# Performance work log

Measured on AMD Instinct MI355X. Metric: run time of the kernel, lower is better.

The kernel has to match this reference:

```python
import jax, jax.numpy as jnp
import numpy as np

B, S, D = 2, 2048, 1024
H = 16
HD = D // H  # 64

def setup_inputs() -> dict:
    key = jax.random.key(0)
    ks = jax.random.split(key, 5)
    scale = 0.02
    x = jax.random.normal(ks[0], (B, S, D), dtype=jnp.float32)
    w_attn = jax.random.normal(ks[1], (D, 3 * D), dtype=jnp.float32) * scale
    b_attn = jnp.zeros((3 * D,), dtype=jnp.float32)
    w_proj = jax.random.normal(ks[2], (D, D), dtype=jnp.float32) * scale
    b_proj = jnp.zeros((D,), dtype=jnp.float32)
    return {"x": x, "w_attn": w_attn, "b_attn": b_attn, "w_proj": w_proj, "b_proj": b_proj}

def reference(x, w_attn, b_attn, w_proj, b_proj):
    b, s, d = x.shape
    qkv = x @ w_attn + b_attn                      # [B,S,3D]
    q, k, v = jnp.split(qkv, 3, axis=-1)
    # [B,H,S,HD]
    q = q.reshape(b, s, H, HD).transpose(0, 2, 1, 3)
    k = k.reshape(b, s, H, HD).transpose(0, 2, 1, 3)
    v = v.reshape(b, s, H, HD).transpose(0, 2, 1, 3)
    scores = jnp.einsum('bhqd,bhkd->bhqk', q, k) * (1.0 / np.sqrt(HD))
    causal = jnp.tril(jnp.ones((s, s), dtype=bool))
    scores = jnp.where(causal[None, None], scores, -jnp.inf)
    attn = jax.nn.softmax(scores, axis=-1)
    out = jnp.einsum('bhqk,bhkd->bhqd', attn, v)   # [B,H,S,HD]
    out = out.transpose(0, 2, 1, 3).reshape(b, s, d)
    return out @ w_proj + b_proj
```

## Files before the change

### kernel.cpp

```cpp
#include <hip/hip_runtime.h>

#define B_  2
#define S_  2048
#define D_  1024
#define H_  16
#define HD_ 64
#define TD_ 3072
#define M_  (B_*S_)
#define NWORK_ 24

using bf16x8 = __attribute__((ext_vector_type(8))) short;
using bf16x4 = __attribute__((ext_vector_type(4))) short;
using f32x4  = __attribute__((ext_vector_type(4))) float;

typedef __attribute__((address_space(1))) unsigned int uint_g;
typedef __attribute__((address_space(3))) unsigned int uint_l;

#define MFMA32 __builtin_amdgcn_mfma_f32_16x16x32_bf16

#if defined(__has_builtin)
#if __has_builtin(__builtin_amdgcn_mfma_f32_16x16x16_bf16_1k)
#define MFMA16(a,b,c) __builtin_amdgcn_mfma_f32_16x16x16_bf16_1k(a,b,c,0,0,0)
#define HAVE_MFMA16 1
#elif __has_builtin(__builtin_amdgcn_mfma_f32_16x16x16bf16_1k)
#define MFMA16(a,b,c) __builtin_amdgcn_mfma_f32_16x16x16bf16_1k(a,b,c,0,0,0)
#define HAVE_MFMA16 1
#endif
#endif
#ifndef HAVE_MFMA16
static __device__ __forceinline__ f32x4 MFMA16_stub(bf16x4 a, bf16x4 b, f32x4 c) { return c; }
#define MFMA16(a,b,c) MFMA16_stub(a,b,c)
#endif

static __device__ __forceinline__ short f2bf(float f) {
    unsigned u = __float_as_uint(f);
    u += 0x7FFFu + ((u >> 16) & 1u);
    return (short)(u >> 16);
}
static __device__ __forceinline__ unsigned pack2bf(float a, float b) {
    return (unsigned)(unsigned short)f2bf(a) | ((unsigned)(unsigned short)f2bf(b) << 16);
}
static __device__ __forceinline__ void gload_lds16(const short* g, short* l) {
    __builtin_amdgcn_global_load_lds((const uint_g*)g, (uint_l*)l, 16, 0, 0);
}
static __device__ __forceinline__ void unpack8(uint4 u, float* f) {
    unsigned a0 = u.x, a1 = u.y, a2 = u.z, a3 = u.w;
    f[0] = __uint_as_float(a0 << 16); f[1] = __uint_as_float(a0 & 0xFFFF0000u);
    f[2] = __uint_as_float(a1 << 16); f[3] = __uint_as_float(a1 & 0xFFFF0000u);
    f[4] = __uint_as_float(a2 << 16); f[5] = __uint_as_float(a2 & 0xFFFF0000u);
    f[6] = __uint_as_float(a3 << 16); f[7] = __uint_as_float(a3 & 0xFFFF0000u);
}

__global__ __launch_bounds__(256)
void prep_kernel(const float* __restrict__ x, short* __restrict__ xb,
                 const float* __restrict__ w_attn, short* __restrict__ wat,
                 const float* __restrict__ w_proj, short* __restrict__ wpt) {
    __shared__ float T[32][33];
    const int bx = blockIdx.x;
    if (bx < 4096) {
        int i = bx * 256 + threadIdx.x;
        float4 v = *((const float4*)x + i);
        short4 o;
        o.x = f2bf(v.x); o.y = f2bf(v.y); o.z = f2bf(v.z); o.w = f2bf(v.w);
        *((short4*)xb + i) = o;
        return;
    }
    const float* W; short* Wt; int N, n0, k0;
    if (bx < 7168) { int b = bx - 4096; W = w_attn; Wt = wat; N = TD_; n0 = (b % 96) * 32; k0 = (b / 96) * 32; }
    else           { int b = bx - 7168; W = w_proj; Wt = wpt; N = D_;  n0 = (b % 32) * 32; k0 = (b / 32) * 32; }
    const int tx = threadIdx.x & 31, ty = threadIdx.x >> 5;
    #pragma unroll
    for (int i = 0; i < 4; ++i)
        T[ty + i * 8][tx] = W[(size_t)(k0 + ty + i * 8) * N + n0 + tx];
    __syncthreads();
    #pragma unroll
    for (int i = 0; i < 4; ++i)
        Wt[(size_t)(n0 + ty + i * 8) * D_ + k0 + tx] = f2bf(T[tx][ty + i * 8]);
}

__global__ __launch_bounds__(256, 3)
void gemm128_qkv_kernel(const short* __restrict__ A, const short* __restrict__ Bt,
                        const float* __restrict__ bias,
                        short* __restrict__ Qo, short* __restrict__ Ko, short* __restrict__ Vto,
                        int M, int N, int K) {
    __shared__ __align__(16) char lds[49152];

    const int tid  = threadIdx.x;
    const int w    = tid >> 6, lane = tid & 63;
    const int quad = lane >> 4, l16 = lane & 15;
    const int wm   = w >> 1,  wn  = w & 1;

    const int gx  = gridDim.x;
    const int nwg = gx * gridDim.y;
    const int bid = blockIdx.y * gx + blockIdx.x;
    const int sbid = (bid & 7) * (nwg >> 3) + (bid >> 3);
    const int rowBase = (sbid / gx) * 128;
    const int colBase = (sbid % gx) * 128;

    const int scol = ((lane & 3) * 8) ^ ((lane & 32) >> 1);
    const int sr0  = w * 32 + (lane >> 2);
    const short* Asrc0 = A  + (size_t)(rowBase + sr0)      * K + scol;
    const short* Asrc1 = A  + (size_t)(rowBase + sr0 + 16) * K + scol;
    const short* Bsrc0 = Bt + (size_t)(colBase + sr0)      * K + scol;
    const short* Bsrc1 = Bt + (size_t)(colBase + sr0 + 16) * K + scol;

    const int rterm = (l16 * 64 + quad * 16) ^ ((l16 & 8) << 2);
    const char* ArdBase = lds + wm * 4096 + rterm;
    const char* BrdBase = lds + 24576 + wn * 4096 + rterm;

#define STAGE_A(t) { int sl_ = ((t) % 3) * 8192; \
    gload_lds16(Asrc0 + (size_t)(t) * 32, (short*)(lds + sl_) + (w * 2)     * 512); \
    gload_lds16(Asrc1 + (size_t)(t) * 32, (short*)(lds + sl_) + (w * 2 + 1) * 512); }
#define STAGE_B(t) { int sl_ = 24576 + ((t) % 3) * 8192; \
    gload_lds16(Bsrc0 + (size_t)(t) * 32, (short*)(lds + sl_) + (w * 2)     * 512); \
    gload_lds16(Bsrc1 + (size_t)(t) * 32, (short*)(lds + sl_) + (w * 2 + 1) * 512); }

    f32x4 acc[4][4];
    const f32x4 zero = {0.f, 0.f, 0.f, 0.f};
    #pragma unroll
    for (int i = 0; i < 4; ++i)
        #pragma unroll
        for (int j = 0; j < 4; ++j) acc[i][j] = zero;

    const int nk = K >> 5;
    STAGE_A(0); STAGE_B(0);
    STAGE_A(1); STAGE_B(1);

    for (int t = 0; t < nk; ++t) {
        if (t + 1 < nk) { asm volatile("s_waitcnt vmcnt(4)" ::: "memory"); }
        else            { asm volatile("s_waitcnt vmcnt(0)" ::: "memory"); }
        __builtin_amdgcn_s_barrier();
        __builtin_amdgcn_sched_barrier(0);

        const int sl = (t % 3) * 8192;
        const char* Ab = ArdBase + sl;
        const char* Bb = BrdBase + sl;
        bf16x8 bfr[4], afr[4];
        #pragma unroll
        for (int ni = 0; ni < 4; ++ni) bfr[ni] = *(const bf16x8*)(Bb + ni * 1024);
        #pragma unroll
        for (int mi = 0; mi < 4; ++mi) afr[mi] = *(const bf16x8*)(Ab + mi * 1024);
        if (t + 2 < nk) { STAGE_A(t + 2); STAGE_B(t + 2); }

        __builtin_amdgcn_s_setprio(1);
        #pragma unroll
        for (int mi = 0; mi < 4; ++mi)
            #pragma unroll
            for (int ni = 0; ni < 4; ++ni)
                acc[mi][ni] = MFMA32(afr[mi], bfr[ni], acc[mi][ni], 0, 0, 0);
        __builtin_amdgcn_s_setprio(0);
    }
#undef STAGE_A
#undef STAGE_B

    #pragma unroll
    for (int ni = 0; ni < 4; ++ni) {
        int col = colBase + wn * 64 + ni * 16 + l16;
        int sel = col >> 10, cr = col & 1023;
        int h = cr >> 6, d = cr & 63;
        float bv  = bias[col];
        if (sel < 2) {
            short* dst = (sel == 0) ? Qo : Ko;
            float  scl = (sel == 0) ? 0.125f * 1.44269504f : 1.0f;
            #pragma unroll
            for (int mi = 0; mi < 4; ++mi) {
                int row = rowBase + wm * 64 + mi * 16 + quad * 4;
                #pragma unroll
                for (int r = 0; r < 4; ++r) {
                    int rw = row + r;
                    int bb = rw >> 11, s = rw & 2047;
                    dst[((size_t)(bb * H_ + h) * S_ + s) * HD_ + d] =
                        f2bf((acc[mi][ni][r] + bv) * scl);
                }
            }
        } else {
            #pragma unroll
            for (int mi = 0; mi < 4; ++mi) {
                int row = rowBase + wm * 64 + mi * 16 + quad * 4;
                int bb = row >> 11, s = row & 2047;
                uint2 o2;
                o2.x = pack2bf(acc[mi][ni][0] + bv, acc[mi][ni][1] + bv);
                o2.y = pack2bf(acc[mi][ni][2] + bv, acc[mi][ni][3] + bv);
                *(uint2*)(Vto + ((size_t)(bb * H_ + h) * HD_ + d) * S_ + s) = o2;
            }
        }
    }
}

__global__ __launch_bounds__(256, 2)
void gemm128_ring_kernel(const short* __restrict__ A, const short* __restrict__ Bt,
                         const float* __restrict__ bias, float* __restrict__ Cf,
                         int M, int N, int K) {
    __shared__ __align__(16) char lds[65536];

    const int tid  = threadIdx.x;
    const int w    = tid >> 6, lane = tid & 63;
    const int quad = lane >> 4, l16 = lane & 15;
    const int wm   = w >> 1,  wn  = w & 1;

    const int gx  = gridDim.x;
    const int nwg = gx * gridDim.y;
    const int bid = blockIdx.y * gx + blockIdx.x;
    const int sbid = (bid & 7) * (nwg >> 3) + (bid >> 3);
    const int rowBase = (sbid / gx) * 128;
    const int colBase = (sbid % gx) * 128;

    const int scol = ((lane & 3) * 8) ^ ((lane & 32) >> 1);
    const int sr0  = w * 32 + (lane >> 2);
    const short* Asrc0 = A  + (size_t)(rowBase + sr0)      * K + scol;
    const short* Asrc1 = A  + (size_t)(rowBase + sr0 + 16) * K + scol;
    const short* Bsrc0 = Bt + (size_t)(colBase + sr0)      * K + scol;
    const short* Bsrc1 = Bt + (size_t)(colBase + sr0 + 16) * K + scol;

    const int rterm = (l16 * 64 + quad * 16) ^ ((l16 & 8) << 2);
    const char* ArdBase = lds + wm * 4096 + rterm;
    const char* BrdBase = lds + 32768 + wn * 4096 + rterm;

#define STAGE_A(t) { int sl_ = ((t) & 3) * 8192; \
    gload_lds16(Asrc0 + (size_t)(t) * 32, (short*)(lds + sl_) + (w * 2)     * 512); \
    gload_lds16(Asrc1 + (size_t)(t) * 32, (short*)(lds + sl_) + (w * 2 + 1) * 512); }
#define STAGE_B(t) { int sl_ = 32768 + ((t) & 3) * 8192; \
    gload_lds16(Bsrc0 + (size_t)(t) * 32, (short*)(lds + sl_) + (w * 2)     * 512); \
    gload_lds16(Bsrc1 + (size_t)(t) * 32, (short*)(lds + sl_) + (w * 2 + 1) * 512); }

    f32x4 acc[4][4];
    const f32x4 zero = {0.f, 0.f, 0.f, 0.f};
    #pragma unroll
    for (int i = 0; i < 4; ++i)
        #pragma unroll
        for (int j = 0; j < 4; ++j) acc[i][j] = zero;

    const int nk = K >> 5;
    STAGE_A(0); STAGE_B(0);
    STAGE_A(1); STAGE_B(1);

    for (int t = 0; t < nk; ++t) {
        if (t + 1 < nk) { asm volatile("s_waitcnt vmcnt(4)" ::: "memory"); }
        else            { asm volatile("s_waitcnt vmcnt(0)" ::: "memory"); }
        __builtin_amdgcn_s_barrier();
        __builtin_amdgcn_sched_barrier(0);

        const char* Ab = ArdBase + (t & 3) * 8192;
        const char* Bb = BrdBase + (t & 3) * 8192;
        bf16x8 bfr[4], afr[4];
        #pragma unroll
        for (int ni = 0; ni < 4; ++ni) bfr[ni] = *(const bf16x8*)(Bb + ni * 1024);
        #pragma unroll
        for (int mi = 0; mi < 4; ++mi) afr[mi] = *(const bf16x8*)(Ab + mi * 1024);
        if (t + 2 < nk) { STAGE_A(t + 2); STAGE_B(t + 2); }

        __builtin_amdgcn_s_setprio(1);
        #pragma unroll
        for (int mi = 0; mi < 4; ++mi)
            #pragma unroll
            for (int ni = 0; ni < 4; ++ni)
                acc[mi][ni] = MFMA32(afr[mi], bfr[ni], acc[mi][ni], 0, 0, 0);
        __builtin_amdgcn_s_setprio(0);
    }
#undef STAGE_A
#undef STAGE_B

    #pragma unroll
    for (int mi = 0; mi < 4; ++mi) {
        int row = rowBase + wm * 64 + mi * 16 + quad * 4;
        #pragma unroll
        for (int ni = 0; ni < 4; ++ni) {
            int col = colBase + wn * 64 + ni * 16 + l16;
            float bv = bias[col];
            #pragma unroll
            for (int r = 0; r < 4; ++r)
                Cf[(size_t)(row + r) * N + col] = acc[mi][ni][r] + bv;
        }
    }
}

__global__ __launch_bounds__(256, 3)
void flash_mfma_kernel(const short* __restrict__ Qg, const short* __restrict__ Kg,
                       const short* __restrict__ Vtg,
                       short* __restrict__ pO, float* __restrict__ pl,
                       short* __restrict__ atb) {
    __shared__ __align__(16) short Ks[64][72];
    __shared__ __align__(16) short Vs[64][72];

    const int plane_id = blockIdx.x;
    const int y = blockIdx.y;
    int qi, kc;
    if (y < 8) { qi = y; kc = 0; }
    else       { qi = 8 + ((y - 8) >> 1); kc = (y - 8) & 1; }
    int nkt = 2 * qi + 2 - kc * 16;
    if (nkt > 16) nkt = 16;
    const int kvOrigin = kc * 1024;

    const int tid  = threadIdx.x;
    const int w    = tid >> 6, lane = tid & 63;
    const int quad = lane >> 4, l16 = lane & 15;
    const int qBase = qi * 128;
    const size_t plane = (size_t)plane_id * S_ * HD_;

    const int sr0 = tid >> 3;
    const int sc0 = (tid & 7) * 8;

    const int qsubA = qBase + w * 32;
    const short* QrowA = Qg + plane + (size_t)(qsubA + l16) * HD_ + quad * 8;
    const bf16x8 qa0 = *(const bf16x8*)(QrowA);
    const bf16x8 qa1 = *(const bf16x8*)(QrowA + 32);
    const short* QrowB = QrowA + 16 * HD_;
    const bf16x8 qb0 = *(const bf16x8*)(QrowB);
    const bf16x8 qb1 = *(const bf16x8*)(QrowB + 32);

    f32x4 oA[4], oB[4];
    const f32x4 zero = {0.f, 0.f, 0.f, 0.f};
    #pragma unroll
    for (int i = 0; i < 4; ++i) { oA[i] = zero; oB[i] = zero; }
    float lA = 0.f, lB = 0.f;
    const int q_globA = qsubA + l16;
    const int q_globB = qsubA + 16 + l16;
    const int q_wave_max = qsubA + 31;

    uint4 ka0, ka1, va0, va1;
    ka0 = *(const uint4*)(Kg  + plane + (size_t)(kvOrigin + sr0)      * HD_ + sc0);
    ka1 = *(const uint4*)(Kg  + plane + (size_t)(kvOrigin + sr0 + 32) * HD_ + sc0);
    va0 = *(const uint4*)(Vtg + plane + (size_t)sr0        * S_ + kvOrigin + sc0);
    va1 = *(const uint4*)(Vtg + plane + (size_t)(sr0 + 32) * S_ + kvOrigin + sc0);

    for (int j = 0; j < nkt; ++j) {
        __syncthreads();
        *(uint4*)&Ks[sr0][sc0]      = ka0;
        *(uint4*)&Ks[sr0 + 32][sc0] = ka1;
        *(uint4*)&Vs[sr0][sc0]      = va0;
        *(uint4*)&Vs[sr0 + 32][sc0] = va1;
        __syncthreads();

        if (j + 1 < nkt) {
            const int kvB = kvOrigin + (j + 1) * 64;
            ka0 = *(const uint4*)(Kg  + plane + (size_t)(kvB + sr0)      * HD_ + sc0);
            ka1 = *(const uint4*)(Kg  + plane + (size_t)(kvB + sr0 + 32) * HD_ + sc0);
            va0 = *(const uint4*)(Vtg + plane + (size_t)sr0        * S_ + kvB + sc0);
            va1 = *(const uint4*)(Vtg + plane + (size_t)(sr0 + 32) * S_ + kvB + sc0);
        }

        const int kvBase = kvOrigin + j * 64;
        if (kvBase > q_wave_max) continue;

        f32x4 sA[4], sB[4];
        __builtin_amdgcn_s_setprio(1);
        #pragma unroll
        for (int ct = 0; ct < 4; ++ct) {
            bf16x8 kf0 = *(const bf16x8*)&Ks[ct * 16 + l16][quad * 8];
            bf16x8 kf1 = *(const bf16x8*)&Ks[ct * 16 + l16][32 + quad * 8];
            f32x4 a = zero, b = zero;
            a = MFMA32(kf0, qa0, a, 0, 0, 0);
            a = MFMA32(kf1, qa1, a, 0, 0, 0);
            b = MFMA32(kf0, qb0, b, 0, 0, 0);
            b = MFMA32(kf1, qb1, b, 0, 0, 0);
            sA[ct] = a; sB[ct] = b;
        }
        __builtin_amdgcn_s_setprio(0);

        if (kvBase + 63 > qsubA) {
            #pragma unroll
            for (int ct = 0; ct < 4; ++ct) {
                int kv = kvBase + ct * 16 + quad * 4;
                #pragma unroll
                for (int r = 0; r < 4; ++r)
                    if (kv + r > q_globA) sA[ct][r] = -3.0e38f;
            }
        }
        if (kvBase + 63 > qsubA + 16) {
            #pragma unroll
            for (int ct = 0; ct < 4; ++ct) {
                int kv = kvBase + ct * 16 + quad * 4;
                #pragma unroll
                for (int r = 0; r < 4; ++r)
                    if (kv + r > q_globB) sB[ct][r] = -3.0e38f;
            }
        }

        #pragma unroll
        for (int ct = 0; ct < 4; ++ct) {
            float pa0 = __builtin_amdgcn_exp2f(sA[ct][0]), pa1 = __builtin_amdgcn_exp2f(sA[ct][1]);
            float pa2 = __builtin_amdgcn_exp2f(sA[ct][2]), pa3 = __builtin_amdgcn_exp2f(sA[ct][3]);
            float pb0 = __builtin_amdgcn_exp2f(sB[ct][0]), pb1 = __builtin_amdgcn_exp2f(sB[ct][1]);
            float pb2 = __builtin_amdgcn_exp2f(sB[ct][2]), pb3 = __builtin_amdgcn_exp2f(sB[ct][3]);
            lA += (pa0 + pa1) + (pa2 + pa3);
            lB += (pb0 + pb1) + (pb2 + pb3);
            bf16x4 pA, pB;
            *(unsigned*)&pA       = pack2bf(pa0, pa1);
            *((unsigned*)&pA + 1) = pack2bf(pa2, pa3);
            *(unsigned*)&pB       = pack2bf(pb0, pb1);
            *((unsigned*)&pB + 1) = pack2bf(pb2, pb3);
            __builtin_amdgcn_s_setprio(1);
            #pragma unroll
            for (int dt = 0; dt < 4; ++dt) {
                bf16x4 vfr = *(const bf16x4*)&Vs[dt * 16 + l16][ct * 16 + quad * 4];
                oA[dt] = MFMA16(vfr, pA, oA[dt]);
                oB[dt] = MFMA16(vfr, pB, oB[dt]);
            }
            __builtin_amdgcn_s_setprio(0);
        }
    }

    lA += __shfl_xor(lA, 16); lA += __shfl_xor(lA, 32);
    lB += __shfl_xor(lB, 16); lB += __shfl_xor(lB, 32);

    if (y < 8) {
        const float invA = 1.0f / lA, invB = 1.0f / lB;
        __syncthreads();
        short* Pw = (w < 2) ? &Ks[w * 32][0] : &Vs[(w - 2) * 32][0];
        #pragma unroll
        for (int dt = 0; dt < 4; ++dt) {
            uint2 ua, ub;
            ua.x = pack2bf(oA[dt][0] * invA, oA[dt][1] * invA);
            ua.y = pack2bf(oA[dt][2] * invA, oA[dt][3] * invA);
            ub.x = pack2bf(oB[dt][0] * invB, oB[dt][1] * invB);
            ub.y = pack2bf(oB[dt][2] * invB, oB[dt][3] * invB);
            *(uint2*)&Pw[l16 * 72 + dt * 16 + quad * 4]        = ua;
            *(uint2*)&Pw[(16 + l16) * 72 + dt * 16 + quad * 4] = ub;
        }
        __builtin_amdgcn_s_waitcnt(0xC07F);
        const int b = plane_id >> 4, h = plane_id & (H_ - 1);
        short* outBase = atb + (size_t)(b * S_ + qBase + w * 32) * D_ + h * HD_;
        #pragma unroll
        for (int pass = 0; pass < 4; ++pass) {
            int r  = pass * 8 + (lane >> 3);
            int cs = (lane & 7) * 8;
            uint4 vv = *(const uint4*)&Pw[r * 72 + cs];
            *(uint4*)(outBase + (size_t)r * D_ + cs) = vv;
        }
        return;
    }

    const size_t lbase = ((size_t)plane_id * NWORK_ + y) * 128 + w * 32;
    if (quad == 0) {
        pl[lbase + l16]      = lA;
        pl[lbase + 16 + l16] = lB;
    }

    __syncthreads();
    short* Pw = (w < 2) ? &Ks[w * 32][0] : &Vs[(w - 2) * 32][0];
    #pragma unroll
    for (int dt = 0; dt < 4; ++dt) {
        uint2 ua, ub;
        ua.x = pack2bf(oA[dt][0], oA[dt][1]);
        ua.y = pack2bf(oA[dt][2], oA[dt][3]);
        ub.x = pack2bf(oB[dt][0], oB[dt][1]);
        ub.y = pack2bf(oB[dt][2], oB[dt][3]);
        *(uint2*)&Pw[l16 * 72 + dt * 16 + quad * 4]        = ua;
        *(uint2*)&Pw[(16 + l16) * 72 + dt * 16 + quad * 4] = ub;
    }
    __builtin_amdgcn_s_waitcnt(0xC07F);
    short* outBase = pO + (((size_t)plane_id * NWORK_ + y) * 128 + w * 32) * 64;
    #pragma unroll
    for (int pass = 0; pass < 4; ++pass) {
        int r  = pass * 8 + (lane >> 3);
        int cs = (lane & 7) * 8;
        uint4 vv = *(const uint4*)&Pw[r * 72 + cs];
        *(uint4*)(outBase + r * 64 + cs) = vv;
    }
}

__global__ __launch_bounds__(256)
void reduce_kernel(const short* __restrict__ pO, const float* __restrict__ pl,
                   short* __restrict__ atb) {
    const int plane_id = blockIdx.x, qi = 8 + blockIdx.y;
    const int h = plane_id & (H_ - 1), b = plane_id >> 4;
    const int tid = threadIdx.x;
    const int row = tid >> 1;
    const int cb  = (tid & 1) * 32;

    const int t0 = 8 + 2 * (qi - 8);

    const size_t pbase = (((size_t)plane_id * NWORK_ + t0) * 128 + row) * 64 + cb;
    float f[32], g[8];
    unpack8(*(const uint4*)(pO + pbase),      f);
    unpack8(*(const uint4*)(pO + pbase + 8),  f + 8);
    unpack8(*(const uint4*)(pO + pbase + 16), f + 16);
    unpack8(*(const uint4*)(pO + pbase + 24), f + 24);
    float l = pl[((size_t)plane_id * NWORK_ + t0) * 128 + row];
    #pragma unroll
    for (int c = 0; c < 4; ++c) {
        unpack8(*(const uint4*)(pO + pbase + 8192 + c * 8), g);
        #pragma unroll
        for (int i = 0; i < 8; ++i) f[c * 8 + i] += g[i];
    }
    l += pl[((size_t)plane_id * NWORK_ + t0 + 1) * 128 + row];

    const float inv = 1.0f / l;
    short* dst = atb + (size_t)(b * S_ + qi * 128 + row) * D_ + h * HD_ + cb;
    #pragma unroll
    for (int c = 0; c < 4; ++c) {
        uint2 o2;
        o2.x = pack2bf(f[c * 8 + 0] * inv, f[c * 8 + 1] * inv);
        o2.y = pack2bf(f[c * 8 + 2] * inv, f[c * 8 + 3] * inv);
        uint2 o3;
        o3.x = pack2bf(f[c * 8 + 4] * inv, f[c * 8 + 5] * inv);
        o3.y = pack2bf(f[c * 8 + 6] * inv, f[c * 8 + 7] * inv);
        uint4 ov; ov.x = o2.x; ov.y = o2.y; ov.z = o3.x; ov.w = o3.y;
        *(uint4*)(dst + c * 8) = ov;
    }
}

extern "C" void kernel_launch(void* const* d_in, const int* in_sizes, int n_in,
                              void* d_out, int out_size, void* d_ws, size_t ws_size,
                              hipStream_t stream) {
    const float* x      = (const float*)d_in[0];
    const float* w_attn = (const float*)d_in[1];
    const float* b_attn = (const float*)d_in[2];
    const float* w_proj = (const float*)d_in[3];
    const float* b_proj = (const float*)d_in[4];
    float* out = (float*)d_out;

    char* ws = (char*)d_ws;
    short* xb  = (short*)ws; ws += (size_t)M_ * D_ * 2;
    short* wat = (short*)ws; ws += (size_t)TD_ * D_ * 2;
    short* wpt = (short*)ws; ws += (size_t)D_ * D_ * 2;
    short* qg  = (short*)ws; ws += (size_t)M_ * D_ * 2;
    short* kg  = (short*)ws; ws += (size_t)M_ * D_ * 2;
    short* vg  = (short*)ws; ws += (size_t)M_ * D_ * 2;
    short* vtg = (short*)ws; ws += (size_t)M_ * D_ * 2;
    short* atb = (short*)ws; ws += (size_t)M_ * D_ * 2;

    short* pO = (short*)d_ws;
    float* pl = (float*)((char*)d_ws + (size_t)32 * NWORK_ * 128 * 64 * 2);

    prep_kernel<<<8192, 256, 0, stream>>>(x, xb, w_attn, wat, w_proj, wpt);

    gemm128_qkv_kernel<<<dim3(TD_ / 128, M_ / 128), 256, 0, stream>>>(
        xb, wat, b_attn, qg, kg, vtg, M_, TD_, D_);

    flash_mfma_kernel<<<dim3(B_ * H_, NWORK_), 256, 0, stream>>>(qg, kg, vtg, pO, pl, atb);

    reduce_kernel<<<dim3(B_ * H_, 8), 256, 0, stream>>>(pO, pl, atb);

    gemm128_ring_kernel<<<dim3(D_ / 128, M_ / 128), 256, 0, stream>>>(
        atb, wpt, b_proj, out, M_, D_, D_);
}
```

Baseline: 172.6 us.

## Triple-buffer K/V tiles with direct global-to-LDS loads and XOR swizzle

Replaces the register-staged K/V double buffering in the flash attention kernel with a three-stage LDS ring filled by direct global-to-LDS loads (gload_lds16), prefetching two tiles ahead and waiting with vmcnt counters. This leaves one barrier per iteration instead of two. LDS rows are unpadded and XOR-swizzled to avoid bank conflicts, and the K/V fragment reads are re-indexed to match. The cost is more LDS per block (48KB), which may limit the 3-blocks-per-CU occupancy target, and correctness depends on the vmcnt accounting and the swizzle math. It also relies on a gload_lds16 helper that must exist outside the lines shown.

```diff
diff --git a/kernel.cpp b/kernel.cpp
--- a/kernel.cpp
+++ b/kernel.cpp
@@ -279,8 +279,7 @@
                        const short* __restrict__ Vtg,
                        short* __restrict__ pO, float* __restrict__ pl,
                        short* __restrict__ atb) {
-    __shared__ __align__(16) short Ks[64][72];
-    __shared__ __align__(16) short Vs[64][72];
+    __shared__ __align__(16) short KV[3][8192];
 
     const int plane_id = blockIdx.x;
     const int y = blockIdx.y;
@@ -297,8 +296,15 @@
     const int qBase = qi * 128;
     const size_t plane = (size_t)plane_id * S_ * HD_;
 
-    const int sr0 = tid >> 3;
-    const int sc0 = (tid & 7) * 8;
+    const int srow = w * 8 + (lane >> 3);
+    const int swz8 = (((lane & 7) ^ (lane >> 3))) * 8;
+
+#define FSTAGE(t) { short* sb_ = &KV[(t) % 3][0]; \
+    const int kvB_ = kvOrigin + (t) * 64; \
+    gload_lds16(Kg  + plane + (size_t)(kvB_ + srow)      * HD_ + swz8, sb_ + (w * 8) * 64); \
+    gload_lds16(Kg  + plane + (size_t)(kvB_ + srow + 32) * HD_ + swz8, sb_ + (32 + w * 8) * 64); \
+    gload_lds16(Vtg + plane + (size_t)srow        * S_ + kvB_ + swz8, sb_ + 4096 + (w * 8) * 64); \
+    gload_lds16(Vtg + plane + (size_t)(srow + 32) * S_ + kvB_ + swz8, sb_ + 4096 + (32 + w * 8) * 64); }
 
     const int qsubA = qBase + w * 32;
     const short* QrowA = Qg + plane + (size_t)(qsubA + l16) * HD_ + quad * 8;
@@ -317,27 +323,19 @@
     const int q_globB = qsubA + 16 + l16;
     const int q_wave_max = qsubA + 31;
 
-    uint4 ka0, ka1, va0, va1;
-    ka0 = *(const uint4*)(Kg  + plane + (size_t)(kvOrigin + sr0)      * HD_ + sc0);
-    ka1 = *(const uint4*)(Kg  + plane + (size_t)(kvOrigin + sr0 + 32) * HD_ + sc0);
-    va0 = *(const uint4*)(Vtg + plane + (size_t)sr0        * S_ + kvOrigin + sc0);
-    va1 = *(const uint4*)(Vtg + plane + (size_t)(sr0 + 32) * S_ + kvOrigin + sc0);
+    const int l7 = l16 & 7;
+
+    FSTAGE(0);
+    if (nkt > 1) FSTAGE(1);
 
     for (int j = 0; j < nkt; ++j) {
-        __syncthreads();
-        *(uint4*)&Ks[sr0][sc0]      = ka0;
-        *(uint4*)&Ks[sr0 + 32][sc0] = ka1;
-        *(uint4*)&Vs[sr0][sc0]      = va0;
-        *(uint4*)&Vs[sr0 + 32][sc0] = va1;
-        __syncthreads();
-
-        if (j + 1 < nkt) {
-            const int kvB = kvOrigin + (j + 1) * 64;
-            ka0 = *(const uint4*)(Kg  + plane + (size_t)(kvB + sr0)      * HD_ + sc0);
-            ka1 = *(const uint4*)(Kg  + plane + (size_t)(kvB + sr0 + 32) * HD_ + sc0);
-            va0 = *(const uint4*)(Vtg + plane + (size_t)sr0        * S_ + kvB + sc0);
-            va1 = *(const uint4*)(Vtg + plane + (size_t)(sr0 + 32) * S_ + kvB + sc0);
-        }
+        if (j + 1 < nkt) { asm volatile("s_waitcnt vmcnt(4)" ::: "memory"); }
+        else             { asm volatile("s_waitcnt vmcnt(0)" ::: "memory"); }
+        __builtin_amdgcn_s_barrier();
+        __builtin_amdgcn_sched_barrier(0);
+
+        const short* sb = &KV[j % 3][0];
+        if (j + 2 < nkt) FSTAGE(j + 2);
 
         const int kvBase = kvOrigin + j * 64;
         if (kvBase > q_wave_max) continue;
@@ -346,8 +344,9 @@
         __builtin_amdgcn_s_setprio(1);
         #pragma unroll
         for (int ct = 0; ct < 4; ++ct) {
-            bf16x8 kf0 = *(const bf16x8*)&Ks[ct * 16 + l16][quad * 8];
-            bf16x8 kf1 = *(const bf16x8*)&Ks[ct * 16 + l16][32 + quad * 8];
+            const short* Krow = sb + (ct * 16 + l16) * 64;
+            bf16x8 kf0 = *(const bf16x8*)(Krow + (quad ^ l7) * 8);
+            bf16x8 kf1 = *(const bf16x8*)(Krow + ((4 + quad) ^ l7) * 8);
             f32x4 a = zero, b = zero;
             a = MFMA32(kf0, qa0, a, 0, 0, 0);
             a = MFMA32(kf1, qa1, a, 0, 0, 0);
@@ -392,7 +391,8 @@
             __builtin_amdgcn_s_setprio(1);
             #pragma unroll
             for (int dt = 0; dt < 4; ++dt) {
-                bf16x4 vfr = *(const bf16x4*)&Vs[dt * 16 + l16][ct * 16 + quad * 4];
+                const short* Vrow = sb + 4096 + (dt * 16 + l16) * 64;
+                bf16x4 vfr = *(const bf16x4*)(Vrow + ((2 * ct + (quad >> 1)) ^ l7) * 8 + (quad & 1) * 4);
                 oA[dt] = MFMA16(vfr, pA, oA[dt]);
                 oB[dt] = MFMA16(vfr, pB, oB[dt]);
             }
@@ -403,10 +403,11 @@
     lA += __shfl_xor(lA, 16); lA += __shfl_xor(lA, 32);
     lB += __shfl_xor(lB, 16); lB += __shfl_xor(lB, 32);
 
+    __syncthreads();
+    short* Pw = &KV[0][0] + w * 2304;
+
     if (y < 8) {
         const float invA = 1.0f / lA, invB = 1.0f / lB;
-        __syncthreads();
-        short* Pw = (w < 2) ? &Ks[w * 32][0] : &Vs[(w - 2) * 32][0];
         #pragma unroll
         for (int dt = 0; dt < 4; ++dt) {
             uint2 ua, ub;
@@ -436,8 +437,6 @@
         pl[lbase + 16 + l16] = lB;
     }
 
-    __syncthreads();
-    short* Pw = (w < 2) ? &Ks[w * 32][0] : &Vs[(w - 2) * 32][0];
     #pragma unroll
     for (int dt = 0; dt < 4; ++dt) {
         uint2 ua, ub;
@@ -457,6 +456,7 @@
         uint4 vv = *(const uint4*)&Pw[r * 72 + cs];
         *(uint4*)(outBase + r * 64 + cs) = vv;
     }
+#undef FSTAGE
 }
 
 __global__ __launch_bounds__(256)
```

Result: slower. 176.8 us (+2.4%).
